# Kernel optimization log

Hardware: AMD Instinct MI355X
Metric: run time of the kernel (lower is better)

## Reference

```python
import jax, jax.numpy as jnp
import numpy as np

PATCH = 8          # patch_size
KEEP_RATIO = 0.7   # keep_ratio at full pruning progress (epoch >= 2*warmup)
MIN_PATCHES = 10


def setup_inputs() -> dict:
    key = jax.random.key(0)
    k_t, k_w1, k_w2 = jax.random.split(key, 3)
    B, H, W, C = 16, 128, 128, 256
    hidden = C // 4
    tokens = jax.random.normal(k_t, (B, H * W, C), dtype=jnp.float32)
    W1 = jax.random.normal(k_w1, (C, hidden), dtype=jnp.float32) * (1.0 / np.sqrt(C))
    b1 = jnp.zeros((hidden,), dtype=jnp.float32)
    W2 = jax.random.normal(k_w2, (hidden, 1), dtype=jnp.float32) * (1.0 / np.sqrt(hidden))
    b2 = jnp.zeros((1,), dtype=jnp.float32)
    return {"tokens": tokens, "W1": W1, "b1": b1, "W2": W2, "b2": b2, "H": H, "W": W}


def reference(tokens, W1, b1, W2, b2, H, W):
    B, N, C = tokens.shape
    ph = pw = PATCH
    nh, nw = H // ph, W // pw              # patches per dim (H,W divisible by PATCH)
    nP = nh * nw

    # ---- unfold into patches: [B, nP, ph*pw, C] (matches torch unfold layout) ----
    x = tokens.reshape(B, nh, ph, nw, pw, C)
    patches_flat = x.transpose(0, 1, 3, 2, 4, 5).reshape(B, nP, ph * pw, C)

    # ---- per-token importance (learnable MLP scorer), mean over patch tokens ----
    h = jax.nn.relu(jnp.einsum('bptc,cd->bptd', patches_flat, W1) + b1)
    tok_imp = jax.nn.sigmoid(jnp.einsum('bptd,do->bpto', h, W2) + b2)[..., 0]  # [B,nP,ph*pw]
    scores = tok_imp.mean(axis=-1)                                             # [B,nP]

    # ---- top-k patch selection, sorted ascending (keeps spatial order) ----
    nK = max(MIN_PATCHES, int(nP * KEEP_RATIO))  # 179 for 256 patches
    _, top_idx = jax.lax.top_k(scores, nK)
    top_idx = jnp.sort(top_idx, axis=-1)         # [B,nK]

    # ---- gather kept patches: [B, nK, ph, pw, C] ----
    patches = patches_flat.reshape(B, nP, ph, pw, C)
    kept = jnp.take_along_axis(patches, top_idx[:, :, None, None, None], axis=1)

    # ---- pad with zero patches to a full nKh x nKw grid, re-assemble 2D map ----
    nKh = -(-nK // nw)            # ceil
    nKw = min(nK, nw)
    pad = nKh * nKw - nK
    kept = jnp.pad(kept, ((0, 0), (0, pad), (0, 0), (0, 0), (0, 0)))
    out2d = kept.reshape(B, nKh, nKw, ph, pw, C).transpose(0, 1, 3, 2, 4, 5)
    H_new, W_new = nKh * ph, nKw * pw
    pruned_tokens = out2d.reshape(B, H_new * W_new, C)
    return pruned_tokens
```

## Files before the change

### kernel.cpp

```cpp
#include <hip/hip_runtime.h>
#include <math.h>

#define CCH   256
#define HID   64
#define MT    256
#define KC    32
#define XT    258
#define NP    256
#define NK    179
#define NSLOT 192
#define IMW   128
#define OUTH  96

__global__ __launch_bounds__(256) void scorer_kernel(
    const float* __restrict__ tokens, const float* __restrict__ W1,
    const float* __restrict__ b1, const float* __restrict__ W2,
    const float* __restrict__ b2v, float* __restrict__ tok_imp)
{
    __shared__ float xs[KC * XT];
    __shared__ float ws[KC * HID];
    __shared__ float red[8 * MT];

    const int t  = threadIdx.x;
    const int tw = t & 31;
    const int hg = t >> 5;
    const long base = (long)blockIdx.x * MT;

    float w2r[8];
    float acc[8][8];
    #pragma unroll
    for (int j = 0; j < 8; ++j) w2r[j] = W2[hg * 8 + j];
    {
        float binit[8];
        #pragma unroll
        for (int j = 0; j < 8; ++j) binit[j] = b1[hg * 8 + j];
        #pragma unroll
        for (int i = 0; i < 8; ++i)
            #pragma unroll
            for (int j = 0; j < 8; ++j) acc[i][j] = binit[j];
    }

    const float4* tok4 = (const float4*)(tokens + base * CCH);
    const int f4k = t & 7;
    const int tl0 = t >> 3;

    for (int ch = 0; ch < CCH / KC; ++ch) {
        #pragma unroll
        for (int pass = 0; pass < 8; ++pass) {
            int tokLocal = tl0 + 32 * pass;
            float4 v = tok4[(long)tokLocal * (CCH / 4) + ch * (KC / 4) + f4k];
            int kloc = f4k * 4;
            xs[(kloc + 0) * XT + tokLocal] = v.x;
            xs[(kloc + 1) * XT + tokLocal] = v.y;
            xs[(kloc + 2) * XT + tokLocal] = v.z;
            xs[(kloc + 3) * XT + tokLocal] = v.w;
        }
        {
            const float4* w14 = (const float4*)(W1 + ch * KC * HID);
            ((float4*)ws)[t]       = w14[t];
            ((float4*)ws)[t + 256] = w14[t + 256];
        }
        __syncthreads();
        #pragma unroll
        for (int kk = 0; kk < KC; ++kk) {
            float xv[8], wv[8];
            #pragma unroll
            for (int i = 0; i < 8; ++i) xv[i] = xs[kk * XT + 32 * i + tw];
            #pragma unroll
            for (int j = 0; j < 8; ++j) wv[j] = ws[kk * HID + hg * 8 + j];
            #pragma unroll
            for (int i = 0; i < 8; ++i)
                #pragma unroll
                for (int j = 0; j < 8; ++j)
                    acc[i][j] = fmaf(xv[i], wv[j], acc[i][j]);
        }
        __syncthreads();
    }

    #pragma unroll
    for (int i = 0; i < 8; ++i) {
        float p = 0.f;
        #pragma unroll
        for (int j = 0; j < 8; ++j) {
            float h = acc[i][j] > 0.f ? acc[i][j] : 0.f;
            p = fmaf(h, w2r[j], p);
        }
        red[hg * MT + tw + 32 * i] = p;
    }
    __syncthreads();
    float s = b2v[0];
    #pragma unroll
    for (int g = 0; g < 8; ++g) s += red[g * MT + t];
    tok_imp[base + t] = 1.f / (1.f + expf(-s));
}

__global__ __launch_bounds__(256) void select_kernel(
    const float* __restrict__ tok_imp, int* __restrict__ sel)
{
    __shared__ float s[NP];
    __shared__ int flag[NP];
    const int b = blockIdx.x, p = threadIdx.x;
    const int ih = p >> 4, iw = p & 15;
    const float* tp = tok_imp + (long)b * 16384 + (ih * 8) * IMW + iw * 8;
    float sum = 0.f;
    #pragma unroll
    for (int ti = 0; ti < 8; ++ti)
        #pragma unroll
        for (int tj = 0; tj < 8; ++tj)
            sum += tp[ti * IMW + tj];
    s[p] = sum;
    __syncthreads();
    const float sp = s[p];
    int rank = 0;
    for (int j = 0; j < NP; ++j) {
        float sj = s[j];
        rank += (sj > sp) || ((sj == sp) && (j < p));
    }
    flag[p] = (rank < NK) ? 1 : 0;
    __syncthreads();
    if (rank < NK) {
        int pos = 0;
        for (int j = 0; j < p; ++j) pos += flag[j];
        sel[b * NK + pos] = p;
    }
}

__global__ __launch_bounds__(256) void gather_kernel(
    const float* __restrict__ tokens, const int* __restrict__ sel,
    float* __restrict__ out)
{
    const int bid = blockIdx.x;
    const int b = bid / NSLOT, k = bid % NSLOT;
    const int t = threadIdx.x;
    const int kh = k >> 4, kw = k & 15;
    float4* dst4 = (float4*)(out + (long)b * OUTH * IMW * CCH);

    if (k >= NK) {
        const float4 z = {0.f, 0.f, 0.f, 0.f};
        #pragma unroll
        for (int i = 0; i < 16; ++i) {
            int f = i * 256 + t;
            int ti = f >> 9;
            int off = f & 511;
            long d = ((long)(kh * 8 + ti) * IMW + kw * 8) * (CCH / 4) + off;
            dst4[d] = z;
        }
        return;
    }
    const int p = sel[b * NK + k];
    const int ih = p >> 4, iw = p & 15;
    const float4* src4 = (const float4*)(tokens + (long)b * 16384 * CCH);
    #pragma unroll
    for (int i = 0; i < 16; ++i) {
        int f = i * 256 + t;
        int ti = f >> 9;
        int off = f & 511;
        long srow = ((long)(ih * 8 + ti) * IMW + iw * 8) * (CCH / 4) + off;
        long drow = ((long)(kh * 8 + ti) * IMW + kw * 8) * (CCH / 4) + off;
        dst4[drow] = src4[srow];
    }
}

extern "C" void kernel_launch(void* const* d_in, const int* in_sizes, int n_in,
                              void* d_out, int out_size, void* d_ws, size_t ws_size,
                              hipStream_t stream)
{
    const float* tokens = (const float*)d_in[0];
    const float* W1     = (const float*)d_in[1];
    const float* b1     = (const float*)d_in[2];
    const float* W2     = (const float*)d_in[3];
    const float* b2     = (const float*)d_in[4];

    const int totalTok = in_sizes[0] / CCH;
    const int B        = totalTok / (IMW * IMW);

    int*   sel     = (int*)d_ws;
    float* tok_imp;
    size_t selBytes = (size_t)B * NK * sizeof(int);
    size_t impBytes = (size_t)totalTok * sizeof(float);
    if (ws_size >= selBytes + 256 + impBytes) {
        tok_imp = (float*)((char*)d_ws + ((selBytes + 255) & ~(size_t)255));
    } else {
        tok_imp = (float*)d_out;
    }

    scorer_kernel<<<totalTok / MT, 256, 0, stream>>>(tokens, W1, b1, W2, b2, tok_imp);
    select_kernel<<<B, 256, 0, stream>>>(tok_imp, sel);
    gather_kernel<<<B * NSLOT, 256, 0, stream>>>(tokens, sel, (float*)d_out);
}
```

Measured before the change: 504.5 us.

## Prefetch scorer tiles into registers, remap LDS reads, ballot-compact selection, nontemporal gather stores

```diff
diff --git a/kernel.cpp b/kernel.cpp
--- a/kernel.cpp
+++ b/kernel.cpp
@@ -12,6 +12,8 @@
 #define IMW   128
 #define OUTH  96
 
+typedef float f32x4 __attribute__((ext_vector_type(4)));
+
 __global__ __launch_bounds__(256) void scorer_kernel(
     const float* __restrict__ tokens, const float* __restrict__ W1,
     const float* __restrict__ b1, const float* __restrict__ W2,
@@ -44,28 +46,46 @@
     const int f4k = t & 7;
     const int tl0 = t >> 3;
 
+    float4 pf[8];
+    #pragma unroll
+    for (int pass = 0; pass < 8; ++pass)
+        pf[pass] = tok4[(long)(tl0 + 32 * pass) * (CCH / 4) + f4k];
+    float4 wpf0 = ((const float4*)W1)[t];
+    float4 wpf1 = ((const float4*)W1)[t + 256];
+
     for (int ch = 0; ch < CCH / KC; ++ch) {
         #pragma unroll
         for (int pass = 0; pass < 8; ++pass) {
             int tokLocal = tl0 + 32 * pass;
-            float4 v = tok4[(long)tokLocal * (CCH / 4) + ch * (KC / 4) + f4k];
+            float4 v = pf[pass];
             int kloc = f4k * 4;
             xs[(kloc + 0) * XT + tokLocal] = v.x;
             xs[(kloc + 1) * XT + tokLocal] = v.y;
             xs[(kloc + 2) * XT + tokLocal] = v.z;
             xs[(kloc + 3) * XT + tokLocal] = v.w;
         }
-        {
-            const float4* w14 = (const float4*)(W1 + ch * KC * HID);
-            ((float4*)ws)[t]       = w14[t];
-            ((float4*)ws)[t + 256] = w14[t + 256];
-        }
+        ((float4*)ws)[t]       = wpf0;
+        ((float4*)ws)[t + 256] = wpf1;
         __syncthreads();
+
+        if (ch < CCH / KC - 1) {
+            #pragma unroll
+            for (int pass = 0; pass < 8; ++pass)
+                pf[pass] = tok4[(long)(tl0 + 32 * pass) * (CCH / 4)
+                                + (ch + 1) * (KC / 4) + f4k];
+            const float4* w14 = (const float4*)(W1 + (ch + 1) * KC * HID);
+            wpf0 = w14[t];
+            wpf1 = w14[t + 256];
+        }
+
         #pragma unroll
         for (int kk = 0; kk < KC; ++kk) {
             float xv[8], wv[8];
             #pragma unroll
-            for (int i = 0; i < 8; ++i) xv[i] = xs[kk * XT + 32 * i + tw];
+            for (int g = 0; g < 4; ++g) {
+                xv[2 * g]     = xs[kk * XT + g * 64 + 2 * tw];
+                xv[2 * g + 1] = xs[kk * XT + g * 64 + 2 * tw + 1];
+            }
             #pragma unroll
             for (int j = 0; j < 8; ++j) wv[j] = ws[kk * HID + hg * 8 + j];
             #pragma unroll
@@ -85,7 +105,9 @@
             float h = acc[i][j] > 0.f ? acc[i][j] : 0.f;
             p = fmaf(h, w2r[j], p);
         }
-        red[hg * MT + tw + 32 * i] = p;
+        int g  = i >> 1;
+        int lt = g * 64 + 2 * tw + (i & 1);
+        red[hg * MT + lt] = p;
     }
     __syncthreads();
     float s = b2v[0];
@@ -98,29 +120,38 @@
     const float* __restrict__ tok_imp, int* __restrict__ sel)
 {
     __shared__ float s[NP];
-    __shared__ int flag[NP];
+    __shared__ unsigned long long wmask[4];
     const int b = blockIdx.x, p = threadIdx.x;
     const int ih = p >> 4, iw = p & 15;
-    const float* tp = tok_imp + (long)b * 16384 + (ih * 8) * IMW + iw * 8;
+    const float4* tp4 = (const float4*)(tok_imp + (long)b * 16384
+                                        + (ih * 8) * IMW + iw * 8);
     float sum = 0.f;
     #pragma unroll
-    for (int ti = 0; ti < 8; ++ti)
-        #pragma unroll
-        for (int tj = 0; tj < 8; ++tj)
-            sum += tp[ti * IMW + tj];
+    for (int ti = 0; ti < 8; ++ti) {
+        float4 a = tp4[ti * (IMW / 4)];
+        float4 c = tp4[ti * (IMW / 4) + 1];
+        sum += a.x; sum += a.y; sum += a.z; sum += a.w;
+        sum += c.x; sum += c.y; sum += c.z; sum += c.w;
+    }
     s[p] = sum;
     __syncthreads();
     const float sp = s[p];
     int rank = 0;
+    #pragma unroll 8
     for (int j = 0; j < NP; ++j) {
         float sj = s[j];
         rank += (sj > sp) || ((sj == sp) && (j < p));
     }
-    flag[p] = (rank < NK) ? 1 : 0;
+    const bool keep = rank < NK;
+    const unsigned long long m = __ballot(keep);
+    const int wv = p >> 6, ln = p & 63;
+    if (ln == 0) wmask[wv] = m;
     __syncthreads();
-    if (rank < NK) {
-        int pos = 0;
-        for (int j = 0; j < p; ++j) pos += flag[j];
+    if (keep) {
+        int pos = __popcll(m & ((1ull << ln) - 1ull));
+        #pragma unroll
+        for (int w = 0; w < 3; ++w)
+            if (w < wv) pos += __popcll(wmask[w]);
         sel[b * NK + pos] = p;
     }
 }
@@ -133,23 +164,23 @@
     const int b = bid / NSLOT, k = bid % NSLOT;
     const int t = threadIdx.x;
     const int kh = k >> 4, kw = k & 15;
-    float4* dst4 = (float4*)(out + (long)b * OUTH * IMW * CCH);
+    f32x4* dst4 = (f32x4*)(out + (long)b * OUTH * IMW * CCH);
 
     if (k >= NK) {
-        const float4 z = {0.f, 0.f, 0.f, 0.f};
+        const f32x4 z = {0.f, 0.f, 0.f, 0.f};
         #pragma unroll
         for (int i = 0; i < 16; ++i) {
             int f = i * 256 + t;
             int ti = f >> 9;
             int off = f & 511;
             long d = ((long)(kh * 8 + ti) * IMW + kw * 8) * (CCH / 4) + off;
-            dst4[d] = z;
+            __builtin_nontemporal_store(z, &dst4[d]);
         }
         return;
     }
     const int p = sel[b * NK + k];
     const int ih = p >> 4, iw = p & 15;
-    const float4* src4 = (const float4*)(tokens + (long)b * 16384 * CCH);
+    const f32x4* src4 = (const f32x4*)(tokens + (long)b * 16384 * CCH);
     #pragma unroll
     for (int i = 0; i < 16; ++i) {
         int f = i * 256 + t;
@@ -157,7 +188,8 @@
         int off = f & 511;
         long srow = ((long)(ih * 8 + ti) * IMW + iw * 8) * (CCH / 4) + off;
         long drow = ((long)(kh * 8 + ti) * IMW + kw * 8) * (CCH / 4) + off;
-        dst4[drow] = src4[srow];
+        f32x4 v = src4[srow];
+        __builtin_nontemporal_store(v, &dst4[drow]);
     }
 }
 
```

New measurement: 482.7 us. 1.05x faster.
